# Kernel optimization log

Measured on AMD Instinct MI355X. Metric: run time of the kernel, lower is better.

Reference implementation:

```python
import jax, jax.numpy as jnp
import numpy as np

NUM_HEADS = 16


def setup_inputs() -> dict:
    key = jax.random.key(0)
    ks = jax.random.split(key, 8)
    b, n, m, L, d = 2, 1024, 4, 1024, 1024
    x = jax.random.normal(ks[0], (b, n, d), dtype=jnp.float32)
    context = jax.random.normal(ks[1], (b, m, L, d), dtype=jnp.float32)
    doc_similarities = jax.random.normal(ks[2], (b, m), dtype=jnp.float32)
    mask = jnp.ones((b, n), dtype=bool)
    context_mask = jnp.ones((b, m, L), dtype=bool)
    Wq = jax.random.normal(ks[3], (d, d), dtype=jnp.float32) * 0.02
    Wkv = jax.random.normal(ks[4], (d, 2 * d), dtype=jnp.float32) * 0.02
    Wout = jax.random.normal(ks[5], (d, d), dtype=jnp.float32) * 0.02
    bout = jnp.zeros((d,), dtype=jnp.float32)
    beta = jnp.ones((), dtype=jnp.float32)
    return {"x": x, "context": context, "doc_similarities": doc_similarities,
            "mask": mask, "context_mask": context_mask,
            "Wq": Wq, "Wkv": Wkv, "Wout": Wout, "bout": bout, "beta": beta}


def reference(x, context, doc_similarities, mask, context_mask, Wq, Wkv, Wout, bout, beta):
    b, n, d = x.shape
    h = NUM_HEADS
    hd = d // h
    _, m, L, _ = context.shape
    kv_len = m * L

    # q projection -> (b, h, n, hd)
    q = (x @ Wq).reshape(b, n, h, hd).transpose(0, 2, 1, 3)

    ctx = context.reshape(b, kv_len, d)
    cmask = context_mask.reshape(b, kv_len)

    # doc similarity bias, broadcast per-token within each doc, scaled by beta
    ds = jnp.repeat(doc_similarities[:, :, None], L, axis=-1).reshape(b, kv_len)
    ds = ds[:, None, None, :] * beta  # (b, 1, 1, kv_len)

    kv = ctx @ Wkv  # (b, kv_len, 2d)
    k, v = jnp.split(kv, 2, axis=-1)
    k = k.reshape(b, kv_len, h, hd).transpose(0, 2, 3, 1)  # (b, h, hd, kv_len)
    v = v.reshape(b, kv_len, h, hd).transpose(0, 2, 1, 3)  # (b, h, kv_len, hd)

    # NOTE: original scales by d**-0.5 (full model dim), not head_size**-0.5
    attention_pre_doc_sim = (q @ k) * (d ** -0.5)  # (b, h, n, kv_len)
    attention = attention_pre_doc_sim + ds

    # faithful mask path: multiply by cross mask, then map exact zeros to -inf
    cross_mask = mask[:, None, :, None] * cmask[:, None, None, :]  # (b,1,n,kv_len)
    attention = attention * cross_mask
    attention = jnp.where(attention == 0.0, -jnp.inf, attention)

    attention_weights = jax.nn.softmax(attention, axis=-1)
    # dropout_rate = 0.0 -> identity

    out = (attention_weights @ v).transpose(0, 2, 1, 3).reshape(b, n, d)
    out = out @ Wout + bout
    return out, attention_pre_doc_sim
```

## Files before the change

### kernel.cpp

```cpp
#include <hip/hip_runtime.h>
#include <cstdint>
#include <cstddef>

typedef unsigned short u16t;
typedef __attribute__((ext_vector_type(4))) float f32x4;
typedef __attribute__((ext_vector_type(4))) int i32x4;
typedef __attribute__((ext_vector_type(8))) __bf16 bf16x8;
typedef __attribute__((ext_vector_type(4))) __bf16 bf16x4;
typedef __attribute__((ext_vector_type(8))) unsigned short u16x8;
typedef __attribute__((ext_vector_type(4))) unsigned short u16x4;

#define INFF __builtin_inff()

__device__ __forceinline__ u16t f2b(float f) {
  union { float f; unsigned u; } x; x.f = f;
  unsigned r = x.u + 0x7FFFu + ((x.u >> 16) & 1u);
  return (u16t)(r >> 16);
}

__device__ __forceinline__ void gload16(const u16t* g, u16t* l) {
  __builtin_amdgcn_global_load_lds((const __attribute__((address_space(1))) void*)g,
                                   (__attribute__((address_space(3))) void*)l, 16, 0, 0);
}

__global__ __launch_bounds__(256) void k_prep(const float* __restrict__ x,
                                              const float* __restrict__ ctx,
                                              u16t* __restrict__ x16,
                                              u16t* __restrict__ ctx16,
                                              const int* __restrict__ cmask,
                                              const float* __restrict__ dsim,
                                              const float* __restrict__ beta_p,
                                              float* __restrict__ biasf) {
  const int bx = blockIdx.x, tid = threadIdx.x;
  if (bx < 2048) {
    int i = bx * 256 + tid;
    f32x4 v = *(const f32x4*)(x + (size_t)i * 4);
    u16x4 o;
    o[0] = f2b(v[0]); o[1] = f2b(v[1]); o[2] = f2b(v[2]); o[3] = f2b(v[3]);
    *(u16x4*)(x16 + (size_t)i * 4) = o;
  } else if (bx < 10240) {
    int i = (bx - 2048) * 256 + tid;
    f32x4 v = *(const f32x4*)(ctx + (size_t)i * 4);
    u16x4 o;
    o[0] = f2b(v[0]); o[1] = f2b(v[1]); o[2] = f2b(v[2]); o[3] = f2b(v[3]);
    *(u16x4*)(ctx16 + (size_t)i * 4) = o;
  } else {
    int idx = (bx - 10240) * 256 + tid;
    int c = idx * 4;
    const float beta = beta_p[0];
    const float ds = dsim[(c >> 12) * 4 + ((c & 4095) >> 10)] * beta;
    i32x4 cm = *(const i32x4*)(cmask + c);
    f32x4 bv;
#pragma unroll
    for (int j = 0; j < 4; ++j) bv[j] = cm[j] ? ds : -INFF;
    *(f32x4*)(biasf + c) = bv;
  }
}

__global__ __launch_bounds__(256) void k_transpose_w3(const float* __restrict__ Wq,
                                                      const float* __restrict__ Wkv,
                                                      const float* __restrict__ Wout,
                                                      u16t* __restrict__ WqT,
                                                      u16t* __restrict__ WkvT,
                                                      u16t* __restrict__ WoutT) {
  __shared__ float tile[64 * 65];
  const int t = threadIdx.x;
  const int bxx = blockIdx.x;
  const float* src; u16t* dst; int C, cb;
  if (bxx < 16)      { src = Wq;   dst = WqT;   C = 1024; cb = bxx * 64; }
  else if (bxx < 48) { src = Wkv;  dst = WkvT;  C = 2048; cb = (bxx - 16) * 64; }
  else               { src = Wout; dst = WoutT; C = 1024; cb = (bxx - 48) * 64; }
  const int rb = blockIdx.y * 64;
#pragma unroll
  for (int it = 0; it < 4; ++it) {
    int c = it * 256 + t;
    int r = c >> 4, ch = c & 15;
    f32x4 v = *(const f32x4*)(src + (size_t)(rb + r) * C + cb + ch * 4);
    float* dp = &tile[r * 65 + ch * 4];
    dp[0] = v[0]; dp[1] = v[1]; dp[2] = v[2]; dp[3] = v[3];
  }
  __syncthreads();
#pragma unroll
  for (int it = 0; it < 2; ++it) {
    int c = it * 256 + t;
    int dr = c >> 3, ch = c & 7;
    u16x8 o;
#pragma unroll
    for (int i = 0; i < 8; ++i) o[i] = f2b(tile[(ch * 8 + i) * 65 + dr]);
    *(u16x8*)(dst + (size_t)(cb + dr) * 1024 + rb + ch * 8) = o;
  }
}

__global__ __launch_bounds__(256) void k_transpose_v(const u16t* __restrict__ kv16,
                                                     u16t* __restrict__ vT) {
  __shared__ u16t tile[64 * 65];
  const int t = threadIdx.x;
  const int kvb = blockIdx.x * 64;
  const int h = blockIdx.y, b = blockIdx.z;
#pragma unroll
  for (int it = 0; it < 2; ++it) {
    int c = it * 256 + t;
    int r = c >> 3, ch = c & 7;
    u16x8 v = *(const u16x8*)(kv16 + (size_t)(b * 4096 + kvb + r) * 2048 + 1024 + h * 64 + ch * 8);
    u16t* dp = &tile[r * 65 + ch * 8];
#pragma unroll
    for (int i = 0; i < 8; ++i) dp[i] = v[i];
  }
  __syncthreads();
#pragma unroll
  for (int it = 0; it < 2; ++it) {
    int c = it * 256 + t;
    int dr = c >> 3, ch = c & 7;
    u16x8 o;
#pragma unroll
    for (int i = 0; i < 8; ++i) o[i] = tile[(ch * 8 + i) * 65 + dr];
    *(u16x8*)(vT + ((size_t)(b * 16 + h) * 64 + dr) * 4096 + kvb + ch * 8) = o;
  }
}

template <int OUTF32, int BIAS>
__global__ __launch_bounds__(256) void k_gemm_bt(const u16t* __restrict__ A,
                                                 const u16t* __restrict__ Bt,
                                                 void* __restrict__ C,
                                                 const float* __restrict__ bias,
                                                 float oscale,
                                                 int K, int lda, int ldb, int ldc, int nbx) {
  __shared__ u16t As[128 * 64];
  __shared__ u16t Bs[128 * 64];
  const int tid = threadIdx.x;
  const int lane = tid & 63, wid = tid >> 6;
  const int l16 = lane & 15, lg = lane >> 4;
  const int wr = wid >> 1, wc = wid & 1;
  const int g = blockIdx.x, per = gridDim.x >> 3;
  const int w = (g & 7) * per + (g >> 3);
  const int bx = w % nbx, by = w / nbx;
  const int brow = by * 128, bcol = bx * 128;
  const int sr = lane >> 3, chs = lane & 7;
  f32x4 acc[4][4] = {};

  for (int k0 = 0; k0 < K; k0 += 64) {
#pragma unroll
    for (int it = 0; it < 4; ++it) {
      int row = it * 32 + wid * 8 + sr;
      int ch = chs ^ (row & 7);
      gload16(A + (size_t)(brow + row) * lda + k0 + ch * 8, &As[it * 2048 + wid * 512]);
      gload16(Bt + (size_t)(bcol + row) * ldb + k0 + ch * 8, &Bs[it * 2048 + wid * 512]);
    }
    __syncthreads();
#pragma unroll
    for (int kk = 0; kk < 2; ++kk) {
      bf16x8 af[4], bfv[4];
#pragma unroll
      for (int mi = 0; mi < 4; ++mi) {
        int row = wr * 64 + mi * 16 + l16;
        int kch = (kk * 4 + lg) ^ (row & 7);
        af[mi] = *(const bf16x8*)(&As[row * 64 + kch * 8]);
      }
#pragma unroll
      for (int ni = 0; ni < 4; ++ni) {
        int row = wc * 64 + ni * 16 + l16;
        int kch = (kk * 4 + lg) ^ (row & 7);
        bfv[ni] = *(const bf16x8*)(&Bs[row * 64 + kch * 8]);
      }
#pragma unroll
      for (int mi = 0; mi < 4; ++mi)
#pragma unroll
        for (int ni = 0; ni < 4; ++ni)
          acc[mi][ni] = __builtin_amdgcn_mfma_f32_16x16x32_bf16(af[mi], bfv[ni], acc[mi][ni], 0, 0, 0);
    }
    __syncthreads();
  }
#pragma unroll
  for (int mi = 0; mi < 4; ++mi) {
#pragma unroll
    for (int ni = 0; ni < 4; ++ni) {
#pragma unroll
      for (int j = 0; j < 4; ++j) {
        size_t row = (size_t)brow + wr * 64 + mi * 16 + lg * 4 + j;
        int col = bcol + wc * 64 + ni * 16 + l16;
        float v = acc[mi][ni][j] * oscale;
        if (BIAS) v += bias[col];
        if (OUTF32)
          __builtin_nontemporal_store(v, (float*)C + row * ldc + col);
        else
          ((u16t*)C)[row * ldc + col] = f2b(v);
      }
    }
  }
}

__global__ __launch_bounds__(256) void k_attn(const u16t* __restrict__ q16,
                                              const u16t* __restrict__ kv16,
                                              const u16t* __restrict__ vT16,
                                              const float* __restrict__ biasf,
                                              const int* __restrict__ mask,
                                              float* __restrict__ pre,
                                              u16t* __restrict__ O16) {
  __shared__ u16t Ks[2][128 * 64];
  __shared__ u16t Vs[2][64 * 128];
  __shared__ u16t Ps[4 * 16 * 128];

  const int tid = threadIdx.x;
  const int lane = tid & 63, wid = tid >> 6;
  const int l16 = lane & 15, lg = lane >> 4;
  const int g = blockIdx.x;
  const int w = (g & 7) * 64 + (g >> 3);
  const int nb = w & 15, hb = w >> 4;
  const int h = hb & 15, b = hb >> 4;
  const int qrow0 = nb * 64 + wid * 16;

  bf16x8 aq0, aq1;
  {
    const u16t* qp = q16 + (size_t)(b * 1024 + qrow0 + l16) * 1024 + h * 64 + lg * 8;
    aq0 = *(const bf16x8*)(qp);
    aq1 = *(const bf16x8*)(qp + 32);
  }
  const bool qm = mask[b * 1024 + qrow0 + l16] != 0;

  float mrow = -INFF, lsum = 0.f;
  f32x4 o[4] = {};

  const u16t* kbase = kv16 + (size_t)b * 4096 * 2048 + (size_t)h * 64;
  const u16t* vbase = vT16 + (size_t)(b * 16 + h) * 64 * 4096;
  float* prerow = pre + (size_t)((b * 16 + h) * 1024 + qrow0 + l16) * 4096;
  const float* biasb = biasf + b * 4096;
  u16t* Pw = &Ps[wid * 2048];
  char* Pwb = (char*)Pw + l16 * 256;
  const int pswz = (l16 & 7) << 4;

  auto stage = [&](int bufi, int kv0s) {
    u16t* Kb = &Ks[bufi][wid * 2048];
    u16t* Vb = &Vs[bufi][wid * 2048];
#pragma unroll
    for (int it = 0; it < 4; ++it) {
      int row = wid * 32 + it * 8 + (lane >> 3);
      int ch = (lane & 7) ^ (row & 7);
      gload16(kbase + (size_t)(kv0s + row) * 2048 + ch * 8, Kb + it * 512);
    }
#pragma unroll
    for (int it = 0; it < 4; ++it) {
      int row = wid * 16 + it * 4 + (lane >> 4);
      int ch = (lane & 15) ^ (row & 7);
      gload16(vbase + (size_t)row * 4096 + kv0s + ch * 8, Vb + it * 512);
    }
  };

  int cur = 0;
  stage(0, 0);
  __syncthreads();

  for (int t = 0; t < 32; ++t) {
    if (t + 1 < 32) stage(cur ^ 1, (t + 1) * 128);
    const u16t* Kc = &Ks[cur][0];
    const u16t* Vc = &Vs[cur][0];
    const int kv0 = t * 128;

    f32x4 s[8];
#pragma unroll
    for (int kb = 0; kb < 8; ++kb) {
      f32x4 acc = {0.f, 0.f, 0.f, 0.f};
      int row = kb * 16 + l16;
      bf16x8 bk0 = *(const bf16x8*)(&Kc[row * 64 + ((lg ^ (row & 7)) << 3)]);
      bf16x8 bk1 = *(const bf16x8*)(&Kc[row * 64 + (((4 + lg) ^ (row & 7)) << 3)]);
      acc = __builtin_amdgcn_mfma_f32_16x16x32_bf16(bk0, aq0, acc, 0, 0, 0);
      acc = __builtin_amdgcn_mfma_f32_16x16x32_bf16(bk1, aq1, acc, 0, 0, 0);
      s[kb] = acc;
    }

    float tmax = -INFF;
#pragma unroll
    for (int kb = 0; kb < 8; ++kb) {
      const int colb = kv0 + kb * 16 + lg * 4;
      __builtin_nontemporal_store(s[kb], (f32x4*)(prerow + colb));
      f32x4 bv = *(const f32x4*)(biasb + colb);
#pragma unroll
      for (int j = 0; j < 4; ++j) {
        float t2 = s[kb][j] + bv[j];
        if (!qm) t2 = 0.f;
        if (t2 == 0.f) t2 = -INFF;
        s[kb][j] = t2;
        tmax = fmaxf(tmax, t2);
      }
    }
    tmax = fmaxf(tmax, __shfl_xor(tmax, 16, 64));
    tmax = fmaxf(tmax, __shfl_xor(tmax, 32, 64));
    const float mold = mrow;
    const float mn = fmaxf(mold, tmax);
    const bool nochange = __all(mn == mold);
    mrow = mn;

    float psum = 0.f;
#pragma unroll
    for (int kb = 0; kb < 8; ++kb) {
      bf16x4 pb;
#pragma unroll
      for (int j = 0; j < 4; ++j) {
        float p = (mn == -INFF) ? 0.f : __expf(s[kb][j] - mn);
        psum += p;
        pb[j] = (__bf16)p;
      }
      *(bf16x4*)(Pwb + ((kb * 32 + lg * 8) ^ pswz)) = pb;
    }
    asm volatile("" ::: "memory");
    psum += __shfl_xor(psum, 16, 64);
    psum += __shfl_xor(psum, 32, 64);

    if (nochange) {
      lsum += psum;
    } else {
      const float fs = (mn == -INFF) ? 0.f : __expf(mold - mn);
      lsum = lsum * fs + psum;
      float fsj[4];
#pragma unroll
      for (int j = 0; j < 4; ++j) fsj[j] = __shfl(fs, lg * 4 + j, 64);
#pragma unroll
      for (int ni = 0; ni < 4; ++ni)
#pragma unroll
        for (int j = 0; j < 4; ++j) o[ni][j] *= fsj[j];
    }

#pragma unroll
    for (int kk2 = 0; kk2 < 4; ++kk2) {
      bf16x8 pa = *(const bf16x8*)(Pwb + ((kk2 * 64 + lg * 16) ^ pswz));
#pragma unroll
      for (int ni = 0; ni < 4; ++ni) {
        int vrow = ni * 16 + l16;
        bf16x8 vb = *(const bf16x8*)(&Vc[vrow * 128 + (((kk2 * 4 + lg) ^ (vrow & 7)) << 3)]);
        o[ni] = __builtin_amdgcn_mfma_f32_16x16x32_bf16(pa, vb, o[ni], 0, 0, 0);
      }
    }
    __syncthreads();
    cur ^= 1;
  }

  float lsj[4];
#pragma unroll
  for (int j = 0; j < 4; ++j) lsj[j] = __shfl(lsum, lg * 4 + j, 64);
#pragma unroll
  for (int ni = 0; ni < 4; ++ni) {
#pragma unroll
    for (int j = 0; j < 4; ++j) {
      size_t row = (size_t)b * 1024 + qrow0 + lg * 4 + j;
      int col = h * 64 + ni * 16 + l16;
      O16[row * 1024 + col] = f2b(o[ni][j] / lsj[j]);
    }
  }
}

extern "C" void kernel_launch(void* const* d_in, const int* in_sizes, int n_in,
                              void* d_out, int out_size, void* d_ws, size_t ws_size,
                              hipStream_t stream) {
  const float* x = (const float*)d_in[0];
  const float* ctx = (const float*)d_in[1];
  const float* dsim = (const float*)d_in[2];
  const int* mask = (const int*)d_in[3];
  const int* cmask = (const int*)d_in[4];
  const float* Wq = (const float*)d_in[5];
  const float* Wkv = (const float*)d_in[6];
  const float* Wout = (const float*)d_in[7];
  const float* bout = (const float*)d_in[8];
  const float* beta = (const float*)d_in[9];

  char* ws = (char*)d_ws;
  u16t* q16 = (u16t*)(ws + (0ull << 20));
  u16t* kv16 = (u16t*)(ws + (4ull << 20));
  u16t* vT16 = (u16t*)(ws + (36ull << 20));
  u16t* O16 = (u16t*)(ws + (52ull << 20));
  u16t* x16 = (u16t*)(ws + (56ull << 20));
  u16t* ctx16 = (u16t*)(ws + (60ull << 20));
  u16t* WqT = (u16t*)(ws + (76ull << 20));
  u16t* WkvT = (u16t*)(ws + (78ull << 20));
  u16t* WoutT = (u16t*)(ws + (82ull << 20));
  float* biasf = (float*)(ws + (84ull << 20));

  float* outp = (float*)d_out;
  float* pre = outp + (size_t)2 * 1024 * 1024;

  k_prep<<<10248, 256, 0, stream>>>(x, ctx, x16, ctx16, cmask, dsim, beta, biasf);
  k_transpose_w3<<<dim3(64, 16), 256, 0, stream>>>(Wq, Wkv, Wout, WqT, WkvT, WoutT);

  k_gemm_bt<0, 0><<<128, 256, 0, stream>>>(x16, WqT, (void*)q16, nullptr, 0.03125f, 1024, 1024, 1024, 1024, 8);
  k_gemm_bt<0, 0><<<1024, 256, 0, stream>>>(ctx16, WkvT, (void*)kv16, nullptr, 1.0f, 1024, 1024, 1024, 2048, 16);
  k_transpose_v<<<dim3(64, 16, 2), 256, 0, stream>>>(kv16, vT16);
  k_attn<<<512, 256, 0, stream>>>(q16, kv16, vT16, biasf, mask, pre, O16);
  k_gemm_bt<1, 1><<<128, 256, 0, stream>>>(O16, WoutT, d_out, bout, 1.0f, 1024, 1024, 1024, 1024, 8);
}
```

Measured before the change: 263.4 us.

## Fuse V transpose into KV GEMM epilogue and relax attention barrier wait

The KV projection GEMM now writes K to a compact buffer and writes V directly in transposed per-head layout from its epilogue, which removes the separate transpose kernel and its extra global round trip. The attention kernel reads K with the new stride. Its end-of-iteration __syncthreads is replaced by a partial vmcnt wait plus s_barrier, so the prefetch for the next tile can stay in flight across the barrier. The transposed stores are 8-byte strided writes and may be less coalesced.

```diff
diff --git a/kernel.cpp b/kernel.cpp
--- a/kernel.cpp
+++ b/kernel.cpp
@@ -91,37 +91,11 @@
   }
 }
 
-__global__ __launch_bounds__(256) void k_transpose_v(const u16t* __restrict__ kv16,
-                                                     u16t* __restrict__ vT) {
-  __shared__ u16t tile[64 * 65];
-  const int t = threadIdx.x;
-  const int kvb = blockIdx.x * 64;
-  const int h = blockIdx.y, b = blockIdx.z;
-#pragma unroll
-  for (int it = 0; it < 2; ++it) {
-    int c = it * 256 + t;
-    int r = c >> 3, ch = c & 7;
-    u16x8 v = *(const u16x8*)(kv16 + (size_t)(b * 4096 + kvb + r) * 2048 + 1024 + h * 64 + ch * 8);
-    u16t* dp = &tile[r * 65 + ch * 8];
-#pragma unroll
-    for (int i = 0; i < 8; ++i) dp[i] = v[i];
-  }
-  __syncthreads();
-#pragma unroll
-  for (int it = 0; it < 2; ++it) {
-    int c = it * 256 + t;
-    int dr = c >> 3, ch = c & 7;
-    u16x8 o;
-#pragma unroll
-    for (int i = 0; i < 8; ++i) o[i] = tile[(ch * 8 + i) * 65 + dr];
-    *(u16x8*)(vT + ((size_t)(b * 16 + h) * 64 + dr) * 4096 + kvb + ch * 8) = o;
-  }
-}
-
-template <int OUTF32, int BIAS>
+template <int MODE>
 __global__ __launch_bounds__(256) void k_gemm_bt(const u16t* __restrict__ A,
                                                  const u16t* __restrict__ Bt,
                                                  void* __restrict__ C,
+                                                 u16t* __restrict__ C2,
                                                  const float* __restrict__ bias,
                                                  float oscale,
                                                  int K, int lda, int ldb, int ldc, int nbx) {
@@ -170,6 +144,24 @@
     }
     __syncthreads();
   }
+
+  if (MODE == 2 && bcol >= 1024) {
+#pragma unroll
+    for (int mi = 0; mi < 4; ++mi) {
+#pragma unroll
+      for (int ni = 0; ni < 4; ++ni) {
+        int vcol = bcol - 1024 + wc * 64 + ni * 16 + l16;
+        int h = vcol >> 6, hd = vcol & 63;
+        int row0 = brow + wr * 64 + mi * 16 + lg * 4;
+        int bb = row0 >> 12, pos = row0 & 4095;
+        u16x4 o4;
+#pragma unroll
+        for (int j = 0; j < 4; ++j) o4[j] = f2b(acc[mi][ni][j]);
+        *(u16x4*)(C2 + ((size_t)((bb * 16 + h) * 64 + hd)) * 4096 + pos) = o4;
+      }
+    }
+    return;
+  }
 #pragma unroll
   for (int mi = 0; mi < 4; ++mi) {
 #pragma unroll
@@ -179,19 +171,20 @@
         size_t row = (size_t)brow + wr * 64 + mi * 16 + lg * 4 + j;
         int col = bcol + wc * 64 + ni * 16 + l16;
         float v = acc[mi][ni][j] * oscale;
-        if (BIAS) v += bias[col];
-        if (OUTF32)
+        if (MODE == 1) {
+          v += bias[col];
           __builtin_nontemporal_store(v, (float*)C + row * ldc + col);
-        else
+        } else {
           ((u16t*)C)[row * ldc + col] = f2b(v);
-      }
-    }
-  }
-}
-
-__global__ __launch_bounds__(256) void k_attn(const u16t* __restrict__ q16,
-                                              const u16t* __restrict__ kv16,
+        }
+      }
+    }
+  }
+}
+
+__global__ __launch_bounds__(256) void k_attn(const u16t* __restrict__ k16,
                                               const u16t* __restrict__ vT16,
+                                              const u16t* __restrict__ q16,
                                               const float* __restrict__ biasf,
                                               const int* __restrict__ mask,
                                               float* __restrict__ pre,
@@ -220,7 +213,7 @@
   float mrow = -INFF, lsum = 0.f;
   f32x4 o[4] = {};
 
-  const u16t* kbase = kv16 + (size_t)b * 4096 * 2048 + (size_t)h * 64;
+  const u16t* kbase = k16 + (size_t)b * 4096 * 1024 + (size_t)h * 64;
   const u16t* vbase = vT16 + (size_t)(b * 16 + h) * 64 * 4096;
   float* prerow = pre + (size_t)((b * 16 + h) * 1024 + qrow0 + l16) * 4096;
   const float* biasb = biasf + b * 4096;
@@ -235,7 +228,7 @@
     for (int it = 0; it < 4; ++it) {
       int row = wid * 32 + it * 8 + (lane >> 3);
       int ch = (lane & 7) ^ (row & 7);
-      gload16(kbase + (size_t)(kv0s + row) * 2048 + ch * 8, Kb + it * 512);
+      gload16(kbase + (size_t)(kv0s + row) * 1024 + ch * 8, Kb + it * 512);
     }
 #pragma unroll
     for (int it = 0; it < 4; ++it) {
@@ -251,6 +244,7 @@
 
   for (int t = 0; t < 32; ++t) {
     if (t + 1 < 32) stage(cur ^ 1, (t + 1) * 128);
+    asm volatile("" ::: "memory");
     const u16t* Kc = &Ks[cur][0];
     const u16t* Vc = &Vs[cur][0];
     const int kv0 = t * 128;
@@ -329,7 +323,11 @@
         o[ni] = __builtin_amdgcn_mfma_f32_16x16x32_bf16(pa, vb, o[ni], 0, 0, 0);
       }
     }
-    __syncthreads();
+
+    asm volatile("s_waitcnt vmcnt(8) lgkmcnt(0)" ::: "memory");
+    __builtin_amdgcn_sched_barrier(0);
+    __builtin_amdgcn_s_barrier();
+    __builtin_amdgcn_sched_barrier(0);
     cur ^= 1;
   }
 
@@ -363,7 +361,7 @@
 
   char* ws = (char*)d_ws;
   u16t* q16 = (u16t*)(ws + (0ull << 20));
-  u16t* kv16 = (u16t*)(ws + (4ull << 20));
+  u16t* k16 = (u16t*)(ws + (4ull << 20));
   u16t* vT16 = (u16t*)(ws + (36ull << 20));
   u16t* O16 = (u16t*)(ws + (52ull << 20));
   u16t* x16 = (u16t*)(ws + (56ull << 20));
@@ -379,9 +377,8 @@
   k_prep<<<10248, 256, 0, stream>>>(x, ctx, x16, ctx16, cmask, dsim, beta, biasf);
   k_transpose_w3<<<dim3(64, 16), 256, 0, stream>>>(Wq, Wkv, Wout, WqT, WkvT, WoutT);
 
-  k_gemm_bt<0, 0><<<128, 256, 0, stream>>>(x16, WqT, (void*)q16, nullptr, 0.03125f, 1024, 1024, 1024, 1024, 8);
-  k_gemm_bt<0, 0><<<1024, 256, 0, stream>>>(ctx16, WkvT, (void*)kv16, nullptr, 1.0f, 1024, 1024, 1024, 2048, 16);
-  k_transpose_v<<<dim3(64, 16, 2), 256, 0, stream>>>(kv16, vT16);
-  k_attn<<<512, 256, 0, stream>>>(q16, kv16, vT16, biasf, mask, pre, O16);
-  k_gemm_bt<1, 1><<<128, 256, 0, stream>>>(O16, WoutT, d_out, bout, 1.0f, 1024, 1024, 1024, 1024, 8);
-}
+  k_gemm_bt<0><<<128, 256, 0, stream>>>(x16, WqT, (void*)q16, nullptr, nullptr, 0.03125f, 1024, 1024, 1024, 1024, 8);
+  k_gemm_bt<2><<<1024, 256, 0, stream>>>(ctx16, WkvT, (void*)k16, vT16, nullptr, 1.0f, 1024, 1024, 1024, 1024, 16);
+  k_attn<<<512, 256, 0, stream>>>(k16, vT16, q16, biasf, mask, pre, O16);
+  k_gemm_bt<1><<<128, 256, 0, stream>>>(O16, WoutT, d_out, nullptr, bout, 1.0f, 1024, 1024, 1024, 1024, 8);
+}
```

Result: no change. 261.9 us (-0.6%).
